# Kernel tuning notes

Measured on AMD Instinct MI355X. Metric: run time of the kernel, lower is better.

## Reference

```python
import jax, jax.numpy as jnp
import numpy as np

B, C, H, W = 32, 512, 32, 32
D = C // 8

def setup_inputs() -> dict:
    key = jax.random.key(0)
    ks = jax.random.split(key, 5)
    return {
        "x": jax.random.normal(ks[0], (B, C, H, W), dtype=jnp.float32),
        "w1": jax.random.normal(ks[1], (D, C), dtype=jnp.float32) * (1.0 / np.sqrt(C)),
        "b1": jax.random.normal(ks[2], (D,), dtype=jnp.float32) * 0.01,
        "w2": jax.random.normal(ks[3], (C, C), dtype=jnp.float32) * (1.0 / np.sqrt(C)),
        "b2": jax.random.normal(ks[4], (C,), dtype=jnp.float32) * 0.01,
    }

def reference(x, w1, b1, w2, b2):
    b, c, h, w = x.shape
    n = h * w
    xf = x.reshape(b, c, n)                                   # [B,C,N]
    # 1x1 convs == channel-mixing GEMMs; conv1 is shared for q and k
    qk = jnp.einsum('bcn,dc->bdn', xf, w1) + b1[None, :, None]  # [B,D,N]
    v = jnp.einsum('bcn,oc->bon', xf, w2) + b2[None, :, None]   # [B,C,N]
    q = qk.transpose(0, 2, 1)                                 # [B,N,D]
    attn = jax.nn.softmax(jnp.einsum('bnd,bdm->bnm', q, qk), axis=-1)  # [B,N,N]
    out = jnp.einsum('bnm,bcm->bnc', attn, v)                 # [B,N,C]
    # Faithful quirk: original views [B,N,C] directly as [B,C,H,W] (no transpose)
    return x + out.reshape(b, c, h, w)
```

## Files before the change

kernel.cpp:

```cpp
#include <hip/hip_runtime.h>
#include <hip/hip_bf16.h>
#include <math.h>

#define B_ 32
#define C_ 512
#define N_ 1024
#define D_ 64
#define OPAD 640

typedef __attribute__((ext_vector_type(4))) float f32x4;
typedef __attribute__((ext_vector_type(4))) float float4v;
typedef __attribute__((ext_vector_type(8))) __bf16 bf16x8;

#define MFMA16(a, b, c) __builtin_amdgcn_mfma_f32_16x16x32_bf16((a), (b), (c), 0, 0, 0)

__device__ inline void load_lds16(const void* g, void* l) {
    __builtin_amdgcn_global_load_lds(
        (const __attribute__((address_space(1))) void*)g,
        (__attribute__((address_space(3))) void*)l, 16, 0, 0);
}

__global__ void k_cast_weights(const float* __restrict__ w1,
                               const float* __restrict__ w2,
                               __hip_bfloat16* __restrict__ Wbf) {
    int idx = blockIdx.x * 256 + threadIdx.x;
    if (idx >= OPAD * C_) return;
    int m = idx >> 9;
    int k = idx & (C_ - 1);
    float val = (m < D_) ? w1[m * C_ + k]
              : (m < D_ + C_) ? w2[(m - D_) * C_ + k] : 0.0f;
    Wbf[idx] = __float2bfloat16(val);
}

__global__ __launch_bounds__(256) void k_transpose_cast(
        const float* __restrict__ x, __hip_bfloat16* __restrict__ xT) {
    __shared__ float tile[64][68];
    int b = blockIdx.z;
    int n0 = blockIdx.x * 64;
    int c0 = blockIdx.y * 64;
    int t = threadIdx.x;
    const float* xb = x + (size_t)b * (C_ * N_);
#pragma unroll
    for (int i = 0; i < 4; i++) {
        int c = i * 16 + (t >> 4);
        int nc = (t & 15) * 4;
        *(float4v*)&tile[c][nc] =
            *(const float4v*)(xb + (size_t)(c0 + c) * N_ + n0 + nc);
    }
    __syncthreads();
    __hip_bfloat16* xTb = xT + (size_t)b * (N_ * C_);
#pragma unroll
    for (int i = 0; i < 2; i++) {
        int n = i * 32 + (t >> 3);
        int cs = (t & 7) * 8;
        alignas(16) __hip_bfloat16 tmp[8];
#pragma unroll
        for (int j = 0; j < 8; j++)
            tmp[j] = __float2bfloat16(tile[cs + j][n]);
        *(bf16x8*)(xTb + (size_t)(n0 + n) * C_ + c0 + cs) = *(bf16x8*)tmp;
    }
}

__global__ __launch_bounds__(256) void k_gemm_qkv(
        const __hip_bfloat16* __restrict__ Wbf,
        const __hip_bfloat16* __restrict__ xT,
        const float* __restrict__ b1, const float* __restrict__ b2,
        __hip_bfloat16* __restrict__ qkT, __hip_bfloat16* __restrict__ v) {
    __shared__ __hip_bfloat16 As[128 * 64];
    __shared__ __hip_bfloat16 Bs[128 * 64];
    __shared__ __hip_bfloat16 epi[4][16][72];
    int b = blockIdx.z;
    int t = threadIdx.x;
    int wave = t >> 6, lane = t & 63, lr = lane & 15, quad = lane >> 4;
    int wm = wave >> 1, wn = wave & 1;
    int m_blk = blockIdx.y * 128;
    int n_blk = blockIdx.x * 128;
    const __hip_bfloat16* xTb = xT + (size_t)b * (N_ * C_);

    f32x4 acc[4][4] = {};
    for (int kk = 0; kk < C_; kk += 64) {
#pragma unroll
        for (int i = 0; i < 4; i++) {
            int id = i * 256 + t;
            int r = id >> 3, cx = id & 7;
            int gc = cx ^ (r & 7);
            load_lds16(Wbf + (size_t)(m_blk + r) * C_ + kk + gc * 8, &As[id * 8]);
            load_lds16(xTb + (size_t)(n_blk + r) * C_ + kk + gc * 8, &Bs[id * 8]);
        }
        __syncthreads();
#pragma unroll
        for (int h = 0; h < 2; h++) {
            bf16x8 af[4], bfr[4];
#pragma unroll
            for (int i = 0; i < 4; i++) {
                int ra = wm * 64 + i * 16 + lr;
                int rb = wn * 64 + i * 16 + lr;
                int q = h * 4 + quad;
                af[i]  = *(const bf16x8*)&As[ra * 64 + (q ^ (lr & 7)) * 8];
                bfr[i] = *(const bf16x8*)&Bs[rb * 64 + (q ^ (lr & 7)) * 8];
            }
#pragma unroll
            for (int mt = 0; mt < 4; mt++)
#pragma unroll
                for (int nt = 0; nt < 4; nt++)
                    acc[mt][nt] = MFMA16(af[mt], bfr[nt], acc[mt][nt]);
        }
        __syncthreads();
    }

#pragma unroll
    for (int mt = 0; mt < 4; mt++) {
        int m_frag = m_blk + wm * 64 + mt * 16;
        if (m_frag >= D_ + C_) continue;
        int m0 = m_frag + quad * 4;
        if (m_frag < D_) {
#pragma unroll
            for (int nt = 0; nt < 4; nt++) {
                int n = n_blk + wn * 64 + nt * 16 + lr;
                alignas(8) __hip_bfloat16 tmp[4];
#pragma unroll
                for (int r = 0; r < 4; r++)
                    tmp[r] = __float2bfloat16(acc[mt][nt][r] + b1[m0 + r]);
                *reinterpret_cast<short4*>(qkT + ((size_t)b * N_ + n) * D_ + m0) =
                    *reinterpret_cast<short4*>(tmp);
            }
        } else {
#pragma unroll
            for (int nt = 0; nt < 4; nt++) {
#pragma unroll
                for (int r = 0; r < 4; r++) {
                    int c = m0 - D_ + r;
                    epi[wave][quad * 4 + r][nt * 16 + lr] =
                        __float2bfloat16(acc[mt][nt][r] + b2[c]);
                }
            }
            int cbase = m_frag - D_;
            int row = lane >> 2;
#pragma unroll
            for (int it = 0; it < 2; it++) {
                int col = it * 32 + (lane & 3) * 8;
                bf16x8 frag = *(const bf16x8*)&epi[wave][row][col];
                *(bf16x8*)(v + (size_t)(b * C_ + cbase + row) * N_
                             + n_blk + wn * 64 + col) = frag;
            }
        }
    }
}

__global__ __launch_bounds__(512, 2) void k_fused_attn(
        const __hip_bfloat16* __restrict__ qkT,
        const __hip_bfloat16* __restrict__ v,
        const float* __restrict__ x, float* __restrict__ out) {
    __shared__ char smem[90112];
    __hip_bfloat16* Ks = (__hip_bfloat16*)smem;
    __hip_bfloat16* Vs = (__hip_bfloat16*)(smem + 8192);
    __hip_bfloat16* Ps = (__hip_bfloat16*)(smem + 73728);
    float* Obuf = (float*)smem;
    __shared__ float Rs[128];

    int b = blockIdx.y;
    int t = threadIdx.x;
    int wave = t >> 6, lane = t & 63, lr = lane & 15, quad = lane >> 4;
    int wm = wave >> 2, wn = wave & 3;
    int n_blk = blockIdx.x * 128;
    const __hip_bfloat16* qb = qkT + (size_t)b * (N_ * D_);
    const __hip_bfloat16* vb = v + (size_t)b * (C_ * N_);

    union bfu { bf16x8 v; __hip_bfloat16 h[8]; };
    bf16x8 bq[2];
    float shift;
    {
        int nq = n_blk + wave * 16 + lr;
        bq[0] = *(const bf16x8*)(qb + (size_t)nq * D_ + quad * 8);
        bq[1] = *(const bf16x8*)(qb + (size_t)nq * D_ + 32 + quad * 8);
        float sq = 0.f;
#pragma unroll
        for (int dh = 0; dh < 2; dh++) {
            bfu u; u.v = bq[dh];
#pragma unroll
            for (int j = 0; j < 8; j++) {
                float qv = __bfloat162float(u.h[j]);
                sq += qv * qv;
            }
        }
        sq += __shfl_xor(sq, 16);
        sq += __shfl_xor(sq, 32);
        shift = sq;
    }

    f32x4 acc[4][8] = {};
    float rsum = 0.f;

    for (int kk = 0; kk < N_; kk += 64) {
        {
            int r = t >> 3, cx = t & 7, gc = cx ^ (r & 7);
            load_lds16(qb + (size_t)(kk + r) * D_ + gc * 8, &Ks[t * 8]);
        }
#pragma unroll
        for (int i = 0; i < 8; i++) {
            int id = i * 512 + t;
            int r = id >> 3, cx = id & 7, gc = cx ^ (r & 7);
            load_lds16(vb + (size_t)r * N_ + kk + gc * 8, &Vs[id * 8]);
        }
        __syncthreads();

#pragma unroll
        for (int mi = 0; mi < 4; mi++) {
            int m = mi * 16 + lr;
            bf16x8 ak0 = *(const bf16x8*)&Ks[m * 64 + ((quad) ^ (lr & 7)) * 8];
            bf16x8 ak1 = *(const bf16x8*)&Ks[m * 64 + ((4 + quad) ^ (lr & 7)) * 8];
            f32x4 s = {};
            s = MFMA16(ak0, bq[0], s);
            s = MFMA16(ak1, bq[1], s);
            alignas(8) __hip_bfloat16 tmp[4];
#pragma unroll
            for (int r = 0; r < 4; r++) {
                float e = __expf(s[r] - shift);
                rsum += e;
                tmp[r] = __float2bfloat16(e);
            }
            int n = wave * 16 + lr;
            int cx2 = mi * 2 + (quad >> 1);
            int slot = cx2 ^ (lr & 7);
            *(short4*)&Ps[n * 64 + slot * 8 + (quad & 1) * 4] = *(short4*)tmp;
        }
        __syncthreads();

#pragma unroll
        for (int h = 0; h < 2; h++) {
            bf16x8 af[4];
#pragma unroll
            for (int i = 0; i < 4; i++) {
                int ra = wm * 64 + i * 16 + lr;
                af[i] = *(const bf16x8*)&Ps[ra * 64 + ((h * 4 + quad) ^ (lr & 7)) * 8];
            }
#pragma unroll
            for (int g = 0; g < 2; g++) {
                bf16x8 bfr[4];
#pragma unroll
                for (int j = 0; j < 4; j++) {
                    int rb = wn * 128 + (g * 4 + j) * 16 + lr;
                    bfr[j] = *(const bf16x8*)&Vs[rb * 64 + ((h * 4 + quad) ^ (lr & 7)) * 8];
                }
#pragma unroll
                for (int mt = 0; mt < 4; mt++)
#pragma unroll
                    for (int j = 0; j < 4; j++)
                        acc[mt][g * 4 + j] = MFMA16(af[mt], bfr[j], acc[mt][g * 4 + j]);
            }
        }
        __syncthreads();
    }

    rsum += __shfl_xor(rsum, 16);
    rsum += __shfl_xor(rsum, 32);
    if (quad == 0) Rs[wave * 16 + lr] = 1.0f / rsum;

    const float* xb = x + (size_t)b * (N_ * C_);
    float* ob = out + (size_t)b * (N_ * C_);
#pragma unroll
    for (int h = 0; h < 2; h++) {
#pragma unroll
        for (int g = 0; g < 2; g++) {
            __syncthreads();
            if (wm == h && (wn >> 1) == g) {
#pragma unroll
                for (int mt = 0; mt < 4; mt++)
#pragma unroll
                    for (int nt = 0; nt < 8; nt++)
#pragma unroll
                        for (int r = 0; r < 4; r++)
                            Obuf[(mt * 16 + quad * 4 + r) * 260
                                 + (wn & 1) * 128 + nt * 16 + lr] =
                                acc[mt][nt][r];
            }
            __syncthreads();
#pragma unroll
            for (int i = 0; i < 8; i++) {
                int id = i * 512 + t;
                int rl = id >> 6;
                int c4 = (id & 63) * 4;
                int n = n_blk + h * 64 + rl;
                float ri = Rs[h * 64 + rl];
                float4v o = *(const float4v*)&Obuf[rl * 260 + c4];
                size_t gidx = (size_t)n * C_ + g * 256 + c4;
                float4v xv = *(const float4v*)(xb + gidx);
                float4v res;
                res.x = xv.x + ri * o.x;
                res.y = xv.y + ri * o.y;
                res.z = xv.z + ri * o.z;
                res.w = xv.w + ri * o.w;
                *(float4v*)(ob + gidx) = res;
            }
        }
    }
}

extern "C" void kernel_launch(void* const* d_in, const int* in_sizes, int n_in,
                              void* d_out, int out_size, void* d_ws, size_t ws_size,
                              hipStream_t stream) {
    const float* x  = (const float*)d_in[0];
    const float* w1 = (const float*)d_in[1];
    const float* b1 = (const float*)d_in[2];
    const float* w2 = (const float*)d_in[3];
    const float* b2 = (const float*)d_in[4];
    float* out = (float*)d_out;

    char* ws = (char*)d_ws;
    size_t off = 0;
    __hip_bfloat16* Wbf = (__hip_bfloat16*)(ws + off); off += (size_t)OPAD * C_ * 2;
    __hip_bfloat16* xT  = (__hip_bfloat16*)(ws + off); off += (size_t)B_ * N_ * C_ * 2;
    __hip_bfloat16* qkT = (__hip_bfloat16*)(ws + off); off += (size_t)B_ * N_ * D_ * 2;
    __hip_bfloat16* v   = (__hip_bfloat16*)(ws + off); off += (size_t)B_ * C_ * N_ * 2;

    hipLaunchKernelGGL(k_cast_weights, dim3((OPAD * C_ + 255) / 256), dim3(256), 0, stream,
                       w1, w2, Wbf);
    hipLaunchKernelGGL(k_transpose_cast, dim3(N_ / 64, C_ / 64, B_), dim3(256), 0, stream,
                       x, xT);
    hipLaunchKernelGGL(k_gemm_qkv, dim3(N_ / 128, OPAD / 128, B_), dim3(256), 0, stream,
                       Wbf, xT, b1, b2, qkT, v);
    hipLaunchKernelGGL(k_fused_attn, dim3(N_ / 128, B_), dim3(512), 0, stream,
                       qkT, v, x, out);
}
```

Measured before the change: 218.3 us.

## Double-buffer V tiles in fused attention and reorder grids batch-fastest

In the fused attention kernel, V tiles are now double-buffered in LDS. The next V tile is prefetched at the start of each iteration, and the next K tile is loaded right after the mid-iteration barrier. This is meant to overlap global-to-LDS traffic with the QK and PV MFMA work instead of stalling on a load-then-sync at the top of every step. LDS use grows to about 152 KB, which limits residency to one block per CU, and Rs moves into the shared buffer. Both the QKV GEMM and the attention grids are also reordered so the batch index is the fastest-varying block dimension.

```diff
diff --git a/kernel.cpp b/kernel.cpp
--- a/kernel.cpp
+++ b/kernel.cpp
@@ -69,12 +69,12 @@
     __shared__ __hip_bfloat16 As[128 * 64];
     __shared__ __hip_bfloat16 Bs[128 * 64];
     __shared__ __hip_bfloat16 epi[4][16][72];
-    int b = blockIdx.z;
+    int b = blockIdx.x;
     int t = threadIdx.x;
     int wave = t >> 6, lane = t & 63, lr = lane & 15, quad = lane >> 4;
     int wm = wave >> 1, wn = wave & 1;
-    int m_blk = blockIdx.y * 128;
-    int n_blk = blockIdx.x * 128;
+    int m_blk = blockIdx.z * 128;
+    int n_blk = blockIdx.y * 128;
     const __hip_bfloat16* xTb = xT + (size_t)b * (N_ * C_);
 
     f32x4 acc[4][4] = {};
@@ -151,20 +151,32 @@
         const __hip_bfloat16* __restrict__ qkT,
         const __hip_bfloat16* __restrict__ v,
         const float* __restrict__ x, float* __restrict__ out) {
-    __shared__ char smem[90112];
-    __hip_bfloat16* Ks = (__hip_bfloat16*)smem;
-    __hip_bfloat16* Vs = (__hip_bfloat16*)(smem + 8192);
-    __hip_bfloat16* Ps = (__hip_bfloat16*)(smem + 73728);
+    __shared__ char smem[155648];
+    __hip_bfloat16* Ks  = (__hip_bfloat16*)smem;
+    __hip_bfloat16* Vs0 = (__hip_bfloat16*)(smem + 8192);
+    __hip_bfloat16* Vs1 = (__hip_bfloat16*)(smem + 73728);
+    __hip_bfloat16* Ps  = (__hip_bfloat16*)(smem + 139264);
     float* Obuf = (float*)smem;
-    __shared__ float Rs[128];
-
-    int b = blockIdx.y;
+    float* Rs   = (float*)(smem + 66560);
+
+    int b = blockIdx.x;
     int t = threadIdx.x;
     int wave = t >> 6, lane = t & 63, lr = lane & 15, quad = lane >> 4;
     int wm = wave >> 2, wn = wave & 3;
-    int n_blk = blockIdx.x * 128;
+    int n_blk = blockIdx.y * 128;
     const __hip_bfloat16* qb = qkT + (size_t)b * (N_ * D_);
     const __hip_bfloat16* vb = v + (size_t)b * (C_ * N_);
+
+    {
+        int r = t >> 3, cxx = t & 7, gc = cxx ^ (r & 7);
+        load_lds16(qb + (size_t)r * D_ + gc * 8, &Ks[t * 8]);
+    }
+#pragma unroll
+    for (int i = 0; i < 8; i++) {
+        int id = i * 512 + t;
+        int r = id >> 3, cxx = id & 7, gc = cxx ^ (r & 7);
+        load_lds16(vb + (size_t)r * N_ + gc * 8, &Vs0[id * 8]);
+    }
 
     union bfu { bf16x8 v; __hip_bfloat16 h[8]; };
     bf16x8 bq[2];
@@ -191,18 +203,21 @@
     f32x4 acc[4][8] = {};
     float rsum = 0.f;
 
-    for (int kk = 0; kk < N_; kk += 64) {
-        {
-            int r = t >> 3, cx = t & 7, gc = cx ^ (r & 7);
-            load_lds16(qb + (size_t)(kk + r) * D_ + gc * 8, &Ks[t * 8]);
-        }
-#pragma unroll
-        for (int i = 0; i < 8; i++) {
-            int id = i * 512 + t;
-            int r = id >> 3, cx = id & 7, gc = cx ^ (r & 7);
-            load_lds16(vb + (size_t)r * N_ + kk + gc * 8, &Vs[id * 8]);
-        }
-        __syncthreads();
+    __syncthreads();
+
+    for (int tt = 0; tt < 16; ++tt) {
+        int kk = tt * 64;
+        __hip_bfloat16* Vcur = (tt & 1) ? Vs1 : Vs0;
+        __hip_bfloat16* Vnxt = (tt & 1) ? Vs0 : Vs1;
+
+        if (tt < 15) {
+#pragma unroll
+            for (int i = 0; i < 8; i++) {
+                int id = i * 512 + t;
+                int r = id >> 3, cxx = id & 7, gc = cxx ^ (r & 7);
+                load_lds16(vb + (size_t)r * N_ + kk + 64 + gc * 8, &Vnxt[id * 8]);
+            }
+        }
 
 #pragma unroll
         for (int mi = 0; mi < 4; mi++) {
@@ -224,7 +239,15 @@
             int slot = cx2 ^ (lr & 7);
             *(short4*)&Ps[n * 64 + slot * 8 + (quad & 1) * 4] = *(short4*)tmp;
         }
-        __syncthreads();
+
+        asm volatile("s_waitcnt lgkmcnt(0)" ::: "memory");
+        __builtin_amdgcn_s_barrier();
+        __builtin_amdgcn_sched_barrier(0);
+
+        if (tt < 15) {
+            int r = t >> 3, cxx = t & 7, gc = cxx ^ (r & 7);
+            load_lds16(qb + (size_t)(kk + 64 + r) * D_ + gc * 8, &Ks[t * 8]);
+        }
 
 #pragma unroll
         for (int h = 0; h < 2; h++) {
@@ -240,7 +263,7 @@
 #pragma unroll
                 for (int j = 0; j < 4; j++) {
                     int rb = wn * 128 + (g * 4 + j) * 16 + lr;
-                    bfr[j] = *(const bf16x8*)&Vs[rb * 64 + ((h * 4 + quad) ^ (lr & 7)) * 8];
+                    bfr[j] = *(const bf16x8*)&Vcur[rb * 64 + ((h * 4 + quad) ^ (lr & 7)) * 8];
                 }
 #pragma unroll
                 for (int mt = 0; mt < 4; mt++)
@@ -317,8 +340,8 @@
                        w1, w2, Wbf);
     hipLaunchKernelGGL(k_transpose_cast, dim3(N_ / 64, C_ / 64, B_), dim3(256), 0, stream,
                        x, xT);
-    hipLaunchKernelGGL(k_gemm_qkv, dim3(N_ / 128, OPAD / 128, B_), dim3(256), 0, stream,
+    hipLaunchKernelGGL(k_gemm_qkv, dim3(B_, N_ / 128, OPAD / 128), dim3(256), 0, stream,
                        Wbf, xT, b1, b2, qkT, v);
-    hipLaunchKernelGGL(k_fused_attn, dim3(N_ / 128, B_), dim3(512), 0, stream,
+    hipLaunchKernelGGL(k_fused_attn, dim3(B_, N_ / 128), dim3(512), 0, stream,
                        qkT, v, x, out);
 }
```

Measured after the change: 207.7 us. 4.9% less time.

## Double-buffer GEMM and attention tiles, fuse weight cast, remap grid by batch

Applied to the files above, without the earlier changes.

The QKV GEMM now double-buffers its A and B LDS tiles so that global-to-LDS loads for the next K slice overlap the MFMA work on the current one. The attention kernel double-buffers the V tiles in LDS and prefetches the next K rows straight into registers instead of staging them in LDS. The weight bf16 cast is folded into the transpose kernel to save a launch. Grids are remapped so batch is the fastest-varying block index, which is meant to keep each batch's blocks on the same XCD for L2 reuse. The cost is that attention LDS grows to about 144KB, which likely allows only one block per CU instead of two.

```diff
diff --git a/kernel.cpp b/kernel.cpp
--- a/kernel.cpp
+++ b/kernel.cpp
@@ -20,25 +20,37 @@
         (__attribute__((address_space(3))) void*)l, 16, 0, 0);
 }
 
-__global__ void k_cast_weights(const float* __restrict__ w1,
-                               const float* __restrict__ w2,
-                               __hip_bfloat16* __restrict__ Wbf) {
-    int idx = blockIdx.x * 256 + threadIdx.x;
-    if (idx >= OPAD * C_) return;
-    int m = idx >> 9;
-    int k = idx & (C_ - 1);
-    float val = (m < D_) ? w1[m * C_ + k]
-              : (m < D_ + C_) ? w2[(m - D_) * C_ + k] : 0.0f;
-    Wbf[idx] = __float2bfloat16(val);
-}
-
 __global__ __launch_bounds__(256) void k_transpose_cast(
-        const float* __restrict__ x, __hip_bfloat16* __restrict__ xT) {
+        const float* __restrict__ x,
+        const float* __restrict__ w1, const float* __restrict__ w2,
+        __hip_bfloat16* __restrict__ xT, __hip_bfloat16* __restrict__ Wbf) {
     __shared__ float tile[64][68];
     int b = blockIdx.z;
     int n0 = blockIdx.x * 64;
     int c0 = blockIdx.y * 64;
     int t = threadIdx.x;
+
+    int lid = blockIdx.x + 16 * blockIdx.y + 128 * blockIdx.z;
+    if (lid < 160) {
+        int base = lid * 2048 + t * 8;
+        int m = base >> 9, k = base & 511;
+        alignas(16) __hip_bfloat16 wtmp[8];
+        if (m < D_ + C_) {
+            const float* s = (m < D_) ? w1 + (size_t)m * C_ + k
+                                      : w2 + (size_t)(m - D_) * C_ + k;
+            float4v a = *(const float4v*)s;
+            float4v c = *(const float4v*)(s + 4);
+            wtmp[0] = __float2bfloat16(a.x); wtmp[1] = __float2bfloat16(a.y);
+            wtmp[2] = __float2bfloat16(a.z); wtmp[3] = __float2bfloat16(a.w);
+            wtmp[4] = __float2bfloat16(c.x); wtmp[5] = __float2bfloat16(c.y);
+            wtmp[6] = __float2bfloat16(c.z); wtmp[7] = __float2bfloat16(c.w);
+        } else {
+#pragma unroll
+            for (int j = 0; j < 8; j++) wtmp[j] = __float2bfloat16(0.0f);
+        }
+        *(bf16x8*)(Wbf + base) = *(bf16x8*)wtmp;
+    }
+
     const float* xb = x + (size_t)b * (C_ * N_);
 #pragma unroll
     for (int i = 0; i < 4; i++) {
@@ -66,28 +78,41 @@
         const __hip_bfloat16* __restrict__ xT,
         const float* __restrict__ b1, const float* __restrict__ b2,
         __hip_bfloat16* __restrict__ qkT, __hip_bfloat16* __restrict__ v) {
-    __shared__ __hip_bfloat16 As[128 * 64];
-    __shared__ __hip_bfloat16 Bs[128 * 64];
-    __shared__ __hip_bfloat16 epi[4][16][72];
-    int b = blockIdx.z;
+    __shared__ __hip_bfloat16 AB[2][2][128 * 64];
+    __hip_bfloat16* epi = &AB[0][0][0];
+    int b = blockIdx.x;
     int t = threadIdx.x;
     int wave = t >> 6, lane = t & 63, lr = lane & 15, quad = lane >> 4;
     int wm = wave >> 1, wn = wave & 1;
-    int m_blk = blockIdx.y * 128;
-    int n_blk = blockIdx.x * 128;
+    int m_blk = blockIdx.z * 128;
+    int n_blk = blockIdx.y * 128;
     const __hip_bfloat16* xTb = xT + (size_t)b * (N_ * C_);
 
+#pragma unroll
+    for (int i = 0; i < 4; i++) {
+        int id = i * 256 + t;
+        int r = id >> 3, cx = id & 7, gc = cx ^ (r & 7);
+        load_lds16(Wbf + (size_t)(m_blk + r) * C_ + gc * 8, &AB[0][0][id * 8]);
+        load_lds16(xTb + (size_t)(n_blk + r) * C_ + gc * 8, &AB[0][1][id * 8]);
+    }
+    __syncthreads();
+
     f32x4 acc[4][4] = {};
-    for (int kk = 0; kk < C_; kk += 64) {
-#pragma unroll
-        for (int i = 0; i < 4; i++) {
-            int id = i * 256 + t;
-            int r = id >> 3, cx = id & 7;
-            int gc = cx ^ (r & 7);
-            load_lds16(Wbf + (size_t)(m_blk + r) * C_ + kk + gc * 8, &As[id * 8]);
-            load_lds16(xTb + (size_t)(n_blk + r) * C_ + kk + gc * 8, &Bs[id * 8]);
-        }
-        __syncthreads();
+    for (int tt = 0; tt < 8; tt++) {
+        const __hip_bfloat16* As = AB[tt & 1][0];
+        const __hip_bfloat16* Bs = AB[tt & 1][1];
+        if (tt < 7) {
+            int kk = (tt + 1) * 64;
+            __hip_bfloat16* An = AB[(tt + 1) & 1][0];
+            __hip_bfloat16* Bn = AB[(tt + 1) & 1][1];
+#pragma unroll
+            for (int i = 0; i < 4; i++) {
+                int id = i * 256 + t;
+                int r = id >> 3, cx = id & 7, gc = cx ^ (r & 7);
+                load_lds16(Wbf + (size_t)(m_blk + r) * C_ + kk + gc * 8, &An[id * 8]);
+                load_lds16(xTb + (size_t)(n_blk + r) * C_ + kk + gc * 8, &Bn[id * 8]);
+            }
+        }
 #pragma unroll
         for (int h = 0; h < 2; h++) {
             bf16x8 af[4], bfr[4];
@@ -130,7 +155,7 @@
 #pragma unroll
                 for (int r = 0; r < 4; r++) {
                     int c = m0 - D_ + r;
-                    epi[wave][quad * 4 + r][nt * 16 + lr] =
+                    epi[(wave * 16 + quad * 4 + r) * 72 + nt * 16 + lr] =
                         __float2bfloat16(acc[mt][nt][r] + b2[c]);
                 }
             }
@@ -139,7 +164,7 @@
 #pragma unroll
             for (int it = 0; it < 2; it++) {
                 int col = it * 32 + (lane & 3) * 8;
-                bf16x8 frag = *(const bf16x8*)&epi[wave][row][col];
+                bf16x8 frag = *(const bf16x8*)&epi[(wave * 16 + row) * 72 + col];
                 *(bf16x8*)(v + (size_t)(b * C_ + cbase + row) * N_
                              + n_blk + wn * 64 + col) = frag;
             }
@@ -151,20 +176,33 @@
         const __hip_bfloat16* __restrict__ qkT,
         const __hip_bfloat16* __restrict__ v,
         const float* __restrict__ x, float* __restrict__ out) {
-    __shared__ char smem[90112];
-    __hip_bfloat16* Ks = (__hip_bfloat16*)smem;
-    __hip_bfloat16* Vs = (__hip_bfloat16*)(smem + 8192);
-    __hip_bfloat16* Ps = (__hip_bfloat16*)(smem + 73728);
+    __shared__ char smem[147456];
+    __hip_bfloat16* Vs0 = (__hip_bfloat16*)smem;
+    __hip_bfloat16* Vs1 = (__hip_bfloat16*)(smem + 65536);
+    __hip_bfloat16* Ps  = (__hip_bfloat16*)(smem + 131072);
     float* Obuf = (float*)smem;
     __shared__ float Rs[128];
 
-    int b = blockIdx.y;
+    int b = blockIdx.x;
     int t = threadIdx.x;
     int wave = t >> 6, lane = t & 63, lr = lane & 15, quad = lane >> 4;
     int wm = wave >> 2, wn = wave & 3;
-    int n_blk = blockIdx.x * 128;
+    int n_blk = blockIdx.y * 128;
     const __hip_bfloat16* qb = qkT + (size_t)b * (N_ * D_);
     const __hip_bfloat16* vb = v + (size_t)b * (C_ * N_);
+
+#pragma unroll
+    for (int i = 0; i < 8; i++) {
+        int id = i * 512 + t;
+        int r = id >> 3, cxx = id & 7, gc = cxx ^ (r & 7);
+        load_lds16(vb + (size_t)r * N_ + gc * 8, &Vs0[id * 8]);
+    }
+    bf16x8 akA[4][2], akB[4][2];
+#pragma unroll
+    for (int mi = 0; mi < 4; mi++) {
+        akA[mi][0] = *(const bf16x8*)(qb + (size_t)(mi * 16 + lr) * D_ + quad * 8);
+        akA[mi][1] = *(const bf16x8*)(qb + (size_t)(mi * 16 + lr) * D_ + 32 + quad * 8);
+    }
 
     union bfu { bf16x8 v; __hip_bfloat16 h[8]; };
     bf16x8 bq[2];
@@ -191,66 +229,81 @@
     f32x4 acc[4][8] = {};
     float rsum = 0.f;
 
-    for (int kk = 0; kk < N_; kk += 64) {
-        {
-            int r = t >> 3, cx = t & 7, gc = cx ^ (r & 7);
-            load_lds16(qb + (size_t)(kk + r) * D_ + gc * 8, &Ks[t * 8]);
-        }
-#pragma unroll
-        for (int i = 0; i < 8; i++) {
-            int id = i * 512 + t;
-            int r = id >> 3, cx = id & 7, gc = cx ^ (r & 7);
-            load_lds16(vb + (size_t)r * N_ + kk + gc * 8, &Vs[id * 8]);
-        }
-        __syncthreads();
-
-#pragma unroll
-        for (int mi = 0; mi < 4; mi++) {
-            int m = mi * 16 + lr;
-            bf16x8 ak0 = *(const bf16x8*)&Ks[m * 64 + ((quad) ^ (lr & 7)) * 8];
-            bf16x8 ak1 = *(const bf16x8*)&Ks[m * 64 + ((4 + quad) ^ (lr & 7)) * 8];
-            f32x4 s = {};
-            s = MFMA16(ak0, bq[0], s);
-            s = MFMA16(ak1, bq[1], s);
-            alignas(8) __hip_bfloat16 tmp[4];
-#pragma unroll
-            for (int r = 0; r < 4; r++) {
-                float e = __expf(s[r] - shift);
-                rsum += e;
-                tmp[r] = __float2bfloat16(e);
-            }
-            int n = wave * 16 + lr;
-            int cx2 = mi * 2 + (quad >> 1);
-            int slot = cx2 ^ (lr & 7);
-            *(short4*)&Ps[n * 64 + slot * 8 + (quad & 1) * 4] = *(short4*)tmp;
-        }
-        __syncthreads();
-
-#pragma unroll
-        for (int h = 0; h < 2; h++) {
-            bf16x8 af[4];
-#pragma unroll
-            for (int i = 0; i < 4; i++) {
-                int ra = wm * 64 + i * 16 + lr;
-                af[i] = *(const bf16x8*)&Ps[ra * 64 + ((h * 4 + quad) ^ (lr & 7)) * 8];
-            }
-#pragma unroll
-            for (int g = 0; g < 2; g++) {
-                bf16x8 bfr[4];
-#pragma unroll
-                for (int j = 0; j < 4; j++) {
-                    int rb = wn * 128 + (g * 4 + j) * 16 + lr;
-                    bfr[j] = *(const bf16x8*)&Vs[rb * 64 + ((h * 4 + quad) ^ (lr & 7)) * 8];
-                }
-#pragma unroll
-                for (int mt = 0; mt < 4; mt++)
-#pragma unroll
-                    for (int j = 0; j < 4; j++)
-                        acc[mt][g * 4 + j] = MFMA16(af[mt], bfr[j], acc[mt][g * 4 + j]);
-            }
-        }
-        __syncthreads();
-    }
+    __syncthreads();
+
+#define ATTN_TILE(TT, VCUR, VNXT, AKC, AKN)                                    \
+    {                                                                          \
+        const int kk = (TT) * 64;                                              \
+        if ((TT) < 15) {                                                       \
+            _Pragma("unroll")                                                  \
+            for (int i = 0; i < 8; i++) {                                      \
+                int id = i * 512 + t;                                          \
+                int r = id >> 3, cxx = id & 7, gc = cxx ^ (r & 7);             \
+                load_lds16(vb + (size_t)r * N_ + kk + 64 + gc * 8,             \
+                           &VNXT[id * 8]);                                     \
+            }                                                                  \
+            _Pragma("unroll")                                                  \
+            for (int mi = 0; mi < 4; mi++) {                                   \
+                AKN[mi][0] = *(const bf16x8*)(qb                               \
+                    + (size_t)(kk + 64 + mi * 16 + lr) * D_ + quad * 8);       \
+                AKN[mi][1] = *(const bf16x8*)(qb                               \
+                    + (size_t)(kk + 64 + mi * 16 + lr) * D_ + 32 + quad * 8);  \
+            }                                                                  \
+        }                                                                      \
+        _Pragma("unroll")                                                      \
+        for (int mi = 0; mi < 4; mi++) {                                       \
+            f32x4 s = {};                                                      \
+            s = MFMA16(AKC[mi][0], bq[0], s);                                  \
+            s = MFMA16(AKC[mi][1], bq[1], s);                                  \
+            alignas(8) __hip_bfloat16 tmp[4];                                  \
+            _Pragma("unroll")                                                  \
+            for (int r = 0; r < 4; r++) {                                      \
+                float e = __expf(s[r] - shift);                                \
+                rsum += e;                                                     \
+                tmp[r] = __float2bfloat16(e);                                  \
+            }                                                                  \
+            int n = wave * 16 + lr;                                            \
+            int cx2 = mi * 2 + (quad >> 1);                                    \
+            int slot = cx2 ^ (lr & 7);                                         \
+            *(short4*)&Ps[n * 64 + slot * 8 + (quad & 1) * 4] = *(short4*)tmp; \
+        }                                                                      \
+        asm volatile("s_waitcnt lgkmcnt(0)" ::: "memory");                     \
+        __builtin_amdgcn_s_barrier();                                          \
+        __builtin_amdgcn_sched_barrier(0);                                     \
+        _Pragma("unroll")                                                      \
+        for (int h = 0; h < 2; h++) {                                          \
+            bf16x8 af[4];                                                      \
+            _Pragma("unroll")                                                  \
+            for (int i = 0; i < 4; i++) {                                      \
+                int ra = wm * 64 + i * 16 + lr;                                \
+                af[i] = *(const bf16x8*)&Ps[ra * 64                            \
+                        + ((h * 4 + quad) ^ (lr & 7)) * 8];                    \
+            }                                                                  \
+            _Pragma("unroll")                                                  \
+            for (int g = 0; g < 2; g++) {                                      \
+                bf16x8 bfr[4];                                                 \
+                _Pragma("unroll")                                              \
+                for (int j = 0; j < 4; j++) {                                  \
+                    int rb = wn * 128 + (g * 4 + j) * 16 + lr;                 \
+                    bfr[j] = *(const bf16x8*)&VCUR[rb * 64                     \
+                             + ((h * 4 + quad) ^ (lr & 7)) * 8];               \
+                }                                                              \
+                _Pragma("unroll")                                              \
+                for (int mt = 0; mt < 4; mt++)                                 \
+                    _Pragma("unroll")                                          \
+                    for (int j = 0; j < 4; j++)                                \
+                        acc[mt][g * 4 + j] =                                   \
+                            MFMA16(af[mt], bfr[j], acc[mt][g * 4 + j]);        \
+            }                                                                  \
+        }                                                                      \
+        __syncthreads();                                                       \
+    }
+
+    for (int tt = 0; tt < 16; tt += 2) {
+        ATTN_TILE(tt,     Vs0, Vs1, akA, akB);
+        ATTN_TILE(tt + 1, Vs1, Vs0, akB, akA);
+    }
+#undef ATTN_TILE
 
     rsum += __shfl_xor(rsum, 16);
     rsum += __shfl_xor(rsum, 32);
@@ -313,12 +366,10 @@
     __hip_bfloat16* qkT = (__hip_bfloat16*)(ws + off); off += (size_t)B_ * N_ * D_ * 2;
     __hip_bfloat16* v   = (__hip_bfloat16*)(ws + off); off += (size_t)B_ * C_ * N_ * 2;
 
-    hipLaunchKernelGGL(k_cast_weights, dim3((OPAD * C_ + 255) / 256), dim3(256), 0, stream,
-                       w1, w2, Wbf);
     hipLaunchKernelGGL(k_transpose_cast, dim3(N_ / 64, C_ / 64, B_), dim3(256), 0, stream,
-                       x, xT);
-    hipLaunchKernelGGL(k_gemm_qkv, dim3(N_ / 128, OPAD / 128, B_), dim3(256), 0, stream,
+                       x, w1, w2, xT, Wbf);
+    hipLaunchKernelGGL(k_gemm_qkv, dim3(B_, N_ / 128, OPAD / 128), dim3(256), 0, stream,
                        Wbf, xT, b1, b2, qkT, v);
-    hipLaunchKernelGGL(k_fused_attn, dim3(N_ / 128, B_), dim3(512), 0, stream,
+    hipLaunchKernelGGL(k_fused_attn, dim3(B_, N_ / 128), dim3(512), 0, stream,
                        qkT, v, x, out);
 }
```

Measured after the change: 327.8 us. 1.5x slower.
